# Kernel optimization log

Measured on AMD Instinct MI355X. Metric: run time of the kernel, lower is better.

## Reference

```python
import jax, jax.numpy as jnp
import numpy as np

EPS = 1e-12  # torch F.normalize eps

def _l2norm(v, axis):
    return v / jnp.maximum(jnp.linalg.norm(v, axis=axis, keepdims=True), EPS)

def setup_inputs() -> dict:
    key = jax.random.key(0)
    k1, k2, k3 = jax.random.split(key, 3)
    N, C, H, W, K = 128, 64, 64, 64, 100
    ALPHA = 100.0
    x = jax.random.normal(k1, (N, C, H, W), dtype=jnp.float32)
    # centroids initialized as F.normalize(rand(K, C)) per __init__
    centroids = jax.random.uniform(k2, (K, C), dtype=jnp.float32)
    centroids = _l2norm(centroids, axis=1)
    # _init_params ties conv weight/bias to centroids (random=False)
    conv_w = 2.0 * ALPHA * centroids                      # [K, C] (1x1 conv kernel)
    conv_b = -ALPHA * jnp.linalg.norm(centroids, axis=1)  # [K]
    return {"x": x, "conv_w": conv_w, "conv_b": conv_b, "centroids": centroids}

def reference(x, conv_w, conv_b, centroids):
    N, C, H, W = x.shape
    K = centroids.shape[0]
    xf = x.reshape(N, C, H * W)                      # [N, C, L]
    # get_assignments: L2-normalize over channels (local copy only)
    x_hat = _l2norm(xf, axis=1)
    logits = jnp.einsum('kc,ncl->nkl', conv_w, x_hat) + conv_b[None, :, None]
    a = jax.nn.softmax(logits, axis=1)               # soft assignment over K
    # residual sum over L expressed as matmul (same math as expand-subtract-sum):
    # vlad[n,k,c] = sum_l a[n,k,l]*xf[n,c,l] - centroids[k,c]*sum_l a[n,k,l]
    agg = jnp.einsum('nkl,ncl->nkc', a, xf)          # note: un-normalized xf, per original code
    vlad = agg - centroids[None] * jnp.sum(a, axis=-1)[..., None]
    # build_vlad (random=False): intra-normalize per cluster, flatten, L2-normalize
    vlad = _l2norm(vlad, axis=2)
    vlad = vlad.reshape(N, K * C)
    vlad = _l2norm(vlad, axis=1)
    # Wrapper applies a final F.normalize (idempotent here but kept for faithfulness)
    vlad = _l2norm(vlad, axis=1)
    return vlad
```

## Files before the change

### kernel.cpp

```cpp
#include <hip/hip_runtime.h>
#include <hip/hip_bf16.h>
#include <cstdint>

#define NB   128
#define CD   64
#define LD   4096
#define KC   100
#define KT   7
#define KR   (KT * 16)
#define AKP  72
#define LSPLIT 8
#define LCH  (LD / LSPLIT)
#define ITERS (LCH / 64)

typedef __attribute__((ext_vector_type(8))) short bf16x8;
typedef __attribute__((ext_vector_type(4))) float f32x4;

__device__ __forceinline__ short bfbits(float f) {
    __hip_bfloat16 h = __float2bfloat16(f);
    return *reinterpret_cast<short*>(&h);
}
__device__ __forceinline__ float bffloat(short s) {
    __hip_bfloat16 h = *reinterpret_cast<__hip_bfloat16*>(&s);
    return __bfloat162float(h);
}

__global__ void k_prep(const float* __restrict__ w, const float* __restrict__ b,
                       uint4* __restrict__ wfrag, float* __restrict__ b_pad)
{
    const int tid = threadIdx.x;
    if (tid < 128) b_pad[tid] = (tid < KC) ? b[tid] : -1e30f;
    if (tid < 64) {
        const int r16 = tid & 15, gg = tid >> 4;
        for (int t = 0; t < KT; ++t) {
            const int k = t * 16 + r16;
            for (int h = 0; h < 2; ++h) {
                short hi8[8], lo8[8];
                for (int j = 0; j < 8; ++j) {
                    const int c = h * 32 + gg * 8 + j;
                    float v = (k < KC) ? w[k * CD + c] : 0.f;
                    short hb = bfbits(v);
                    hi8[j] = hb;
                    lo8[j] = bfbits(v - bffloat(hb));
                }
                wfrag[((t * 2 + h) * 2 + 0) * 64 + tid] = *reinterpret_cast<uint4*>(hi8);
                wfrag[((t * 2 + h) * 2 + 1) * 64 + tid] = *reinterpret_cast<uint4*>(lo8);
            }
        }
    }
}

__global__ __launch_bounds__(256, 2) void k_fused(
    const float* __restrict__ x, const uint4* __restrict__ wfrag,
    const float* __restrict__ b_pad,
    float* __restrict__ agg_pT, float* __restrict__ asum_pT, int n0)
{
    __shared__ float xs[CD][65];
    __shared__ __align__(16) __hip_bfloat16 akl[KR][AKP];
    __shared__ __align__(16) uint4 wlds[KT * 2 * 2 * 64];

    const int tid  = threadIdx.x;
    const int lane = tid & 63;
    const int wv   = tid >> 6;
    const int lloc = lane & 15;
    const int g    = lane >> 4;

    for (int i = tid; i < KT * 2 * 2 * 64; i += 256) wlds[i] = wfrag[i];

    const int nn = blockIdx.x >> 3;
    const int ls = blockIdx.x & 7;
    const int n  = n0 + nn;
    const float* xb = x + (size_t)n * CD * LD + ls * LCH;

    const float4* bp4 = reinterpret_cast<const float4*>(b_pad);
    float4 bv[KT];
#pragma unroll
    for (int t = 0; t < KT; ++t) bv[t] = bp4[t * 4 + g];

    f32x4 aagg[KT];
#pragma unroll
    for (int mt = 0; mt < KT; ++mt) aagg[mt] = (f32x4){0.f, 0.f, 0.f, 0.f};
    float asl = 0.f;

    float4 pv[4];
#pragma unroll
    for (int i = 0; i < 4; ++i) {
        int idx = tid + i * 256, c = idx >> 4, lq = idx & 15;
        pv[i] = *reinterpret_cast<const float4*>(xb + (size_t)c * LD + lq * 4);
    }

    const bf16x8* wfp = reinterpret_cast<const bf16x8*>(wlds);
    const int lw = wv * 16 + lloc;
    const int cb = wv * 16 + lloc;

    for (int it = 0; it < ITERS; ++it) {
        __syncthreads();
#pragma unroll
        for (int i = 0; i < 4; ++i) {
            int idx = tid + i * 256, c = idx >> 4, lq = idx & 15;
            xs[c][lq * 4 + 0] = pv[i].x; xs[c][lq * 4 + 1] = pv[i].y;
            xs[c][lq * 4 + 2] = pv[i].z; xs[c][lq * 4 + 3] = pv[i].w;
        }
        __syncthreads();

        float ss = 0.f;
        bf16x8 bhi0, blo0, bhi1, blo1;
#pragma unroll
        for (int j = 0; j < 8; ++j) {
            float v0 = xs[g * 8 + j][lw];
            ss = fmaf(v0, v0, ss);
            short h0 = bfbits(v0);
            bhi0[j] = h0; blo0[j] = bfbits(v0 - bffloat(h0));
            float v1 = xs[32 + g * 8 + j][lw];
            ss = fmaf(v1, v1, ss);
            short h1 = bfbits(v1);
            bhi1[j] = h1; blo1[j] = bfbits(v1 - bffloat(h1));
        }
        ss += __shfl_xor(ss, 16);
        ss += __shfl_xor(ss, 32);
        const float rn = 1.0f / fmaxf(sqrtf(ss), 1e-12f);

        f32x4 acc[KT];
#pragma unroll
        for (int t = 0; t < KT; ++t) acc[t] = (f32x4){0.f, 0.f, 0.f, 0.f};
#pragma unroll
        for (int t = 0; t < KT; ++t) {
            bf16x8 wh0 = wfp[((t * 2 + 0) * 2 + 0) * 64 + lane];
            bf16x8 wl0 = wfp[((t * 2 + 0) * 2 + 1) * 64 + lane];
            bf16x8 wh1 = wfp[((t * 2 + 1) * 2 + 0) * 64 + lane];
            bf16x8 wl1 = wfp[((t * 2 + 1) * 2 + 1) * 64 + lane];
            acc[t] = __builtin_amdgcn_mfma_f32_16x16x32_bf16(wh0, bhi0, acc[t], 0, 0, 0);
            acc[t] = __builtin_amdgcn_mfma_f32_16x16x32_bf16(wh1, bhi1, acc[t], 0, 0, 0);
            acc[t] = __builtin_amdgcn_mfma_f32_16x16x32_bf16(wh0, blo0, acc[t], 0, 0, 0);
            acc[t] = __builtin_amdgcn_mfma_f32_16x16x32_bf16(wh1, blo1, acc[t], 0, 0, 0);
            acc[t] = __builtin_amdgcn_mfma_f32_16x16x32_bf16(wl0, bhi0, acc[t], 0, 0, 0);
            acc[t] = __builtin_amdgcn_mfma_f32_16x16x32_bf16(wl1, bhi1, acc[t], 0, 0, 0);
        }

        float m = -3.0e38f;
#pragma unroll
        for (int t = 0; t < KT; ++t) {
            acc[t][0] = fmaf(acc[t][0], rn, bv[t].x);
            acc[t][1] = fmaf(acc[t][1], rn, bv[t].y);
            acc[t][2] = fmaf(acc[t][2], rn, bv[t].z);
            acc[t][3] = fmaf(acc[t][3], rn, bv[t].w);
            m = fmaxf(m, fmaxf(fmaxf(acc[t][0], acc[t][1]), fmaxf(acc[t][2], acc[t][3])));
        }
        m = fmaxf(m, __shfl_xor(m, 16));
        m = fmaxf(m, __shfl_xor(m, 32));
        float s = 0.f;
#pragma unroll
        for (int t = 0; t < KT; ++t) {
#pragma unroll
            for (int r = 0; r < 4; ++r) {
                float e = __expf(acc[t][r] - m);
                acc[t][r] = e;
                s += e;
            }
        }
        s += __shfl_xor(s, 16);
        s += __shfl_xor(s, 32);
        const float inv = 1.0f / s;

#pragma unroll
        for (int r = 0; r < 4; ++r) {
#pragma unroll
            for (int t = 0; t < KT; ++t)
                akl[t * 16 + g * 4 + r][lw] = __float2bfloat16(acc[t][r] * inv);
        }

        if (it + 1 < ITERS) {
#pragma unroll
            for (int i = 0; i < 4; ++i) {
                int idx = tid + i * 256, c = idx >> 4, lq = idx & 15;
                pv[i] = *reinterpret_cast<const float4*>(
                    xb + (it + 1) * 64 + (size_t)c * LD + lq * 4);
            }
        }
        __syncthreads();

        if (tid < KR) {
            const bf16x8* rp = reinterpret_cast<const bf16x8*>(&akl[tid][0]);
            float rs = 0.f;
#pragma unroll
            for (int q = 0; q < 8; ++q) {
                bf16x8 v = rp[q];
#pragma unroll
                for (int j = 0; j < 8; ++j) rs += bffloat(v[j]);
            }
            asl += rs;
        }

#pragma unroll
        for (int h = 0; h < 2; ++h) {
            const float* xrow = &xs[cb][h * 32 + g * 8];
            bf16x8 xh, xl;
#pragma unroll
            for (int j = 0; j < 8; ++j) {
                float v = xrow[j];
                short hb = bfbits(v);
                xh[j] = hb; xl[j] = bfbits(v - bffloat(hb));
            }
#pragma unroll
            for (int mt = 0; mt < KT; ++mt) {
                bf16x8 af = *reinterpret_cast<const bf16x8*>(
                    &akl[mt * 16 + lloc][h * 32 + g * 8]);
                aagg[mt] = __builtin_amdgcn_mfma_f32_16x16x32_bf16(af, xh, aagg[mt], 0, 0, 0);
                aagg[mt] = __builtin_amdgcn_mfma_f32_16x16x32_bf16(af, xl, aagg[mt], 0, 0, 0);
            }
        }
    }

    const size_t nls = (size_t)nn * LSPLIT + ls;
    float* ap = agg_pT + (nls * 64 + cb) * 128 + g * 4;
#pragma unroll
    for (int mt = 0; mt < KT; ++mt)
        *reinterpret_cast<f32x4*>(ap + mt * 16) = aagg[mt];
    if (tid < KR) asum_pT[nls * KR + tid] = asl;
}

__global__ __launch_bounds__(256, 1) void k_final(
    const float* __restrict__ agg_pT, const float* __restrict__ asum_pT,
    const float* __restrict__ cent, float* __restrict__ out, int n0)
{
    __shared__ float vbuf[KC][65];
    __shared__ float asum_s[KR];
    __shared__ float rn_s[KC];
    __shared__ float red[256];

    const int tid = threadIdx.x;
    const int nn  = blockIdx.x;
    const int n   = n0 + nn;
    const size_t nb8 = (size_t)nn * LSPLIT;

    if (tid < KR) {
        float s = 0.f;
#pragma unroll
        for (int ls = 0; ls < LSPLIT; ++ls)
            s += asum_pT[(nb8 + ls) * KR + tid];
        asum_s[tid] = s;
    }
    __syncthreads();

    for (int idx = tid; idx < 64 * 128; idx += 256) {
        int c = idx >> 7, k = idx & 127;
        if (k < KC) {
            float s = 0.f;
#pragma unroll
            for (int ls = 0; ls < LSPLIT; ++ls)
                s += agg_pT[((nb8 + ls) * 64 + c) * 128 + k];
            vbuf[k][c] = fmaf(-cent[k * CD + c], asum_s[k], s);
        }
    }
    __syncthreads();

    if (tid < KC) {
        float ssq = 0.f;
#pragma unroll 8
        for (int c = 0; c < CD; ++c) {
            float v = vbuf[tid][c];
            ssq = fmaf(v, v, ssq);
        }
        rn_s[tid] = 1.0f / fmaxf(sqrtf(ssq), 1e-12f);
    }
    __syncthreads();

    float gp = 0.f;
    for (int idx = tid; idx < KC * CD; idx += 256) {
        int k = idx >> 6, c = idx & 63;
        float v = vbuf[k][c] * rn_s[k];
        gp = fmaf(v, v, gp);
    }
    red[tid] = gp;
    __syncthreads();
    for (int off = 128; off > 0; off >>= 1) {
        if (tid < off) red[tid] += red[tid + off];
        __syncthreads();
    }
    const float gnorm = 1.0f / fmaxf(sqrtf(red[0]), 1e-12f);

    float* op = out + (size_t)n * (KC * CD);
    for (int idx = tid; idx < KC * CD; idx += 256) {
        int k = idx >> 6, c = idx & 63;
        op[idx] = vbuf[k][c] * rn_s[k] * gnorm;
    }
}

extern "C" void kernel_launch(void* const* d_in, const int* in_sizes, int n_in,
                              void* d_out, int out_size, void* d_ws, size_t ws_size,
                              hipStream_t stream)
{
    const float* x  = (const float*)d_in[0];
    const float* w  = (const float*)d_in[1];
    const float* b  = (const float*)d_in[2];
    const float* ct = (const float*)d_in[3];
    float* out = (float*)d_out;

    char* wsp = (char*)d_ws;
    uint4* wfrag = (uint4*)wsp;
    float* b_pad = (float*)(wsp + 28672);
    char* chunk  = wsp + 32768;

    const size_t agg_per_n  = (size_t)LSPLIT * 64 * 128 * 4;
    const size_t asum_per_n = (size_t)LSPLIT * KR * 4;
    const size_t per_n = agg_per_n + asum_per_n;

    size_t avail = ws_size > 32768 ? ws_size - 32768 : 0;
    int nc = (int)(avail / per_n);
    if (nc < 1) nc = 1;
    if (nc > NB) nc = NB;

    float* agg_pT  = (float*)chunk;
    float* asum_pT = (float*)(chunk + agg_per_n * (size_t)nc);

    k_prep<<<1, 128, 0, stream>>>(w, b, wfrag, b_pad);
    for (int n0 = 0; n0 < NB; n0 += nc) {
        int cn = NB - n0; if (cn > nc) cn = nc;
        k_fused<<<cn * LSPLIT, 256, 0, stream>>>(x, wfrag, b_pad, agg_pT, asum_pT, n0);
        k_final<<<cn, 256, 0, stream>>>(agg_pT, asum_pT, ct, out, n0);
    }
}
```

Before: 98.24 us.

## Drop LDS staging of x tile and read directly from global memory

Removes the shared-memory x tile and its register prefetch pipeline. Each thread now reads its x columns straight from global memory for the logits pass and reads rows again with float4 loads for the aggregation pass, so the data comes twice through cache. The freed LDS and registers allow raising launch bounds to 3 blocks per CU. The cost is uncoalesced strided column reads, no prefetch overlap, and duplicate global traffic.

Result: no change. 100.1 us (+1.9%).

```diff
diff --git a/kernel.cpp b/kernel.cpp
--- a/kernel.cpp
+++ b/kernel.cpp
@@ -50,12 +50,11 @@
     }
 }
 
-__global__ __launch_bounds__(256, 2) void k_fused(
+__global__ __launch_bounds__(256, 3) void k_fused(
     const float* __restrict__ x, const uint4* __restrict__ wfrag,
     const float* __restrict__ b_pad,
     float* __restrict__ agg_pT, float* __restrict__ asum_pT, int n0)
 {
-    __shared__ float xs[CD][65];
     __shared__ __align__(16) __hip_bfloat16 akl[KR][AKP];
     __shared__ __align__(16) uint4 wlds[KT * 2 * 2 * 64];
 
@@ -82,36 +81,23 @@
     for (int mt = 0; mt < KT; ++mt) aagg[mt] = (f32x4){0.f, 0.f, 0.f, 0.f};
     float asl = 0.f;
 
-    float4 pv[4];
-#pragma unroll
-    for (int i = 0; i < 4; ++i) {
-        int idx = tid + i * 256, c = idx >> 4, lq = idx & 15;
-        pv[i] = *reinterpret_cast<const float4*>(xb + (size_t)c * LD + lq * 4);
-    }
-
     const bf16x8* wfp = reinterpret_cast<const bf16x8*>(wlds);
     const int lw = wv * 16 + lloc;
     const int cb = wv * 16 + lloc;
 
+    __syncthreads();
+
     for (int it = 0; it < ITERS; ++it) {
-        __syncthreads();
-#pragma unroll
-        for (int i = 0; i < 4; ++i) {
-            int idx = tid + i * 256, c = idx >> 4, lq = idx & 15;
-            xs[c][lq * 4 + 0] = pv[i].x; xs[c][lq * 4 + 1] = pv[i].y;
-            xs[c][lq * 4 + 2] = pv[i].z; xs[c][lq * 4 + 3] = pv[i].w;
-        }
-        __syncthreads();
-
+        const float* xcol = xb + it * 64 + lw;
         float ss = 0.f;
         bf16x8 bhi0, blo0, bhi1, blo1;
 #pragma unroll
         for (int j = 0; j < 8; ++j) {
-            float v0 = xs[g * 8 + j][lw];
+            float v0 = xcol[(size_t)(g * 8 + j) * LD];
             ss = fmaf(v0, v0, ss);
             short h0 = bfbits(v0);
             bhi0[j] = h0; blo0[j] = bfbits(v0 - bffloat(h0));
-            float v1 = xs[32 + g * 8 + j][lw];
+            float v1 = xcol[(size_t)(32 + g * 8 + j) * LD];
             ss = fmaf(v1, v1, ss);
             short h1 = bfbits(v1);
             bhi1[j] = h1; blo1[j] = bfbits(v1 - bffloat(h1));
@@ -162,20 +148,13 @@
         s += __shfl_xor(s, 32);
         const float inv = 1.0f / s;
 
+        __syncthreads();
+
 #pragma unroll
         for (int r = 0; r < 4; ++r) {
 #pragma unroll
             for (int t = 0; t < KT; ++t)
                 akl[t * 16 + g * 4 + r][lw] = __float2bfloat16(acc[t][r] * inv);
-        }
-
-        if (it + 1 < ITERS) {
-#pragma unroll
-            for (int i = 0; i < 4; ++i) {
-                int idx = tid + i * 256, c = idx >> 4, lq = idx & 15;
-                pv[i] = *reinterpret_cast<const float4*>(
-                    xb + (it + 1) * 64 + (size_t)c * LD + lq * 4);
-            }
         }
         __syncthreads();
 
@@ -193,11 +172,14 @@
 
 #pragma unroll
         for (int h = 0; h < 2; ++h) {
-            const float* xrow = &xs[cb][h * 32 + g * 8];
+            const float* xrow = xb + (size_t)cb * LD + it * 64 + h * 32 + g * 8;
+            float4 xr0 = *reinterpret_cast<const float4*>(xrow);
+            float4 xr1 = *reinterpret_cast<const float4*>(xrow + 4);
+            float xv8[8] = {xr0.x, xr0.y, xr0.z, xr0.w, xr1.x, xr1.y, xr1.z, xr1.w};
             bf16x8 xh, xl;
 #pragma unroll
             for (int j = 0; j < 8; ++j) {
-                float v = xrow[j];
+                float v = xv8[j];
                 short hb = bfbits(v);
                 xh[j] = hb; xl[j] = bfbits(v - bffloat(hb));
             }
```
